# Kernel optimization log

Measured on AMD Instinct MI355X. Metric: run time of the kernel, lower is better.

Reference implementation:

```python
import jax, jax.numpy as jnp
import numpy as np

C = 64
INTER = C // 2  # 32
B, L = 4, 4096


def setup_inputs() -> dict:
    key = jax.random.key(0)
    ks = jax.random.split(key, 9)
    s_in = 1.0 / np.sqrt(C)
    s_inter = 1.0 / np.sqrt(INTER)
    return {
        "x": jax.random.normal(ks[0], (B, C, L), dtype=jnp.float32),
        "g_w": jax.random.normal(ks[1], (INTER, C), dtype=jnp.float32) * s_in,
        "g_b": jax.random.normal(ks[2], (INTER,), dtype=jnp.float32) * s_in,
        "theta_w": jax.random.normal(ks[3], (INTER, C), dtype=jnp.float32) * s_in,
        "theta_b": jax.random.normal(ks[4], (INTER,), dtype=jnp.float32) * s_in,
        "phi_w": jax.random.normal(ks[5], (INTER, C), dtype=jnp.float32) * s_in,
        "phi_b": jax.random.normal(ks[6], (INTER,), dtype=jnp.float32) * s_in,
        # NOTE: original inits W to zero (residual starts as identity); we use small
        # random values so the reference exercises the full computation.
        "W_w": jax.random.normal(ks[7], (C, INTER), dtype=jnp.float32) * s_inter,
        "W_b": jax.random.normal(ks[8], (C,), dtype=jnp.float32) * s_inter,
    }


def reference(x, g_w, g_b, theta_w, theta_b, phi_w, phi_b, W_w, W_b):
    # 1x1 Conv1d == channel matmul: [O,C] x [B,C,L] -> [B,O,L]
    g_x = jnp.einsum('oc,bcl->bol', g_w, x) + g_b[None, :, None]
    theta_x = jnp.einsum('oc,bcl->bol', theta_w, x) + theta_b[None, :, None]
    phi_x = jnp.einsum('oc,bcl->bol', phi_w, x) + phi_b[None, :, None]
    # f[b,l,m] = theta[:,l] . phi[:,m]  (unscaled attention scores, [B,L,L])
    f = jnp.einsum('bol,bom->blm', theta_x, phi_x)
    f_div_C = jax.nn.softmax(f, axis=-1)
    # y[b,o,l] = sum_m f[b,l,m] * g[b,o,m]
    y = jnp.einsum('blm,bom->bol', f_div_C, g_x)
    W_y = jnp.einsum('co,bol->bcl', W_w, y) + W_b[None, :, None]
    return W_y + x
```

## Files before the change

kernel.cpp:

```cpp
#include <hip/hip_runtime.h>

#define Bn 4
#define Cdim 64
#define INTER 32
#define Ln 4096
#define LOG2E 1.44269504088896340736f

typedef _Float16 half_t;
typedef __attribute__((ext_vector_type(8))) _Float16 half8v;
typedef __attribute__((ext_vector_type(4))) short short4v;
typedef __attribute__((ext_vector_type(8))) short short8v;
typedef __attribute__((ext_vector_type(4))) float f32x4;

__device__ __forceinline__ unsigned short f2bf(float f) {
    unsigned u = __float_as_uint(f);
    u += 0x7fffu + ((u >> 16) & 1u);
    return (unsigned short)(u >> 16);
}
__device__ __forceinline__ float bf2f(unsigned short b) {
    return __uint_as_float(((unsigned)b) << 16);
}
__device__ __forceinline__ unsigned pack_bf(float a, float b) {
    unsigned ua = __float_as_uint(a) + 0x8000u;
    unsigned ub = __float_as_uint(b) + 0x8000u;
    return __builtin_amdgcn_perm(ub, ua, 0x07060302);
}
__device__ __forceinline__ void gll16(const void* g, void* l) {
    __builtin_amdgcn_global_load_lds(
        (const __attribute__((address_space(1))) unsigned int*)g,
        (__attribute__((address_space(3))) unsigned int*)l, 16, 0, 0);
}

__global__ void setup_kernel(const float* __restrict__ g_w, const float* __restrict__ g_b,
                             const float* __restrict__ th_w, const float* __restrict__ th_b,
                             const float* __restrict__ ph_w, const float* __restrict__ ph_b,
                             const float* __restrict__ W_w, const float* __restrict__ W_b,
                             half_t* __restrict__ Wcat, float* __restrict__ biasbuf,
                             float* __restrict__ bc, half_t* __restrict__ Wm) {
    int blk = blockIdx.x, tid = threadIdx.x;
    if (blk < 96) {
        int row = blk;
        float v;
        if (row < 32) v = th_w[row * 64 + tid] * LOG2E;
        else if (row < 64) v = ph_w[(row - 32) * 64 + tid];
        else v = g_w[(row - 64) * 64 + tid];
        Wcat[row * 64 + tid] = (half_t)v;
    } else if (blk == 96) {
        for (int i = tid; i < 96; i += 64) {
            float v = (i < 32) ? th_b[i] * LOG2E : (i < 64) ? ph_b[i - 32] : g_b[i - 64];
            biasbuf[i] = v;
        }
    } else if (blk == 97) {
        bc[tid] = W_b[tid];
    } else {
        int l15 = tid & 15, jb = (tid >> 4) * 8;
        for (int mf = 0; mf < 4; mf++) {
            int c = mf * 16 + l15;
            half_t tmp[8];
            for (int j = 0; j < 8; j++) tmp[j] = (half_t)W_w[c * 32 + jb + j];
            float4 v;
            __builtin_memcpy(&v, tmp, 16);
            *(float4*)(Wm + (mf * 64 + tid) * 8) = v;
        }
    }
}

__global__ __launch_bounds__(192) void proj_kernel(
        const float* __restrict__ x, const half_t* __restrict__ Wcat,
        const float* __restrict__ biasbuf,
        half_t* __restrict__ thfrag, half_t* __restrict__ phfrag,
        unsigned short* __restrict__ gfrag) {
    __shared__ half_t sx[64][72];
    __shared__ unsigned short sg[2048];
    int tid = threadIdx.x;
    int b = blockIdx.x >> 6;
    int l0 = (blockIdx.x & 63) << 6;

    for (int i = tid; i < 1024; i += 192) {
        int c = i >> 4, lq = (i & 15) << 2;
        float4 v = *(const float4*)&x[(size_t)(b * 64 + c) * Ln + l0 + lq];
        sx[lq + 0][c] = (half_t)v.x;
        sx[lq + 1][c] = (half_t)v.y;
        sx[lq + 2][c] = (half_t)v.z;
        sx[lq + 3][c] = (half_t)v.w;
    }
    __syncthreads();

    int lane = tid & 63, grp = tid >> 6;
    int l15 = lane & 15, quad = lane >> 4;

    half8v wA[2][2];
#pragma unroll
    for (int mf = 0; mf < 2; mf++)
#pragma unroll
        for (int kk = 0; kk < 2; kk++)
            wA[mf][kk] = *(const half8v*)(Wcat + (grp * 32 + mf * 16 + l15) * 64 +
                                          kk * 32 + quad * 8);
    half8v xB[4][2];
#pragma unroll
    for (int nf = 0; nf < 4; nf++)
#pragma unroll
        for (int kk = 0; kk < 2; kk++)
            xB[nf][kk] = *(const half8v*)&sx[nf * 16 + l15][kk * 32 + quad * 8];

    f32x4 acc[2][4];
    const f32x4 z = {0.f, 0.f, 0.f, 0.f};
#pragma unroll
    for (int mf = 0; mf < 2; mf++)
#pragma unroll
        for (int nf = 0; nf < 4; nf++) {
            f32x4 a = __builtin_amdgcn_mfma_f32_16x16x32_f16(wA[mf][0], xB[nf][0], z, 0, 0, 0);
            acc[mf][nf] = __builtin_amdgcn_mfma_f32_16x16x32_f16(wA[mf][1], xB[nf][1], a, 0, 0, 0);
        }
#pragma unroll
    for (int mf = 0; mf < 2; mf++) {
        float4 bv = *(const float4*)&biasbuf[grp * 32 + mf * 16 + quad * 4];
#pragma unroll
        for (int nf = 0; nf < 4; nf++) {
            acc[mf][nf][0] += bv.x; acc[mf][nf][1] += bv.y;
            acc[mf][nf][2] += bv.z; acc[mf][nf][3] += bv.w;
        }
    }

    if (grp < 2) {
        half_t* F = (grp == 0) ? thfrag : phfrag;
#pragma unroll
        for (int mf = 0; mf < 2; mf++)
#pragma unroll
            for (int nf = 0; nf < 4; nf++) {
                half_t h[4];
                h[0] = (half_t)acc[mf][nf][0]; h[1] = (half_t)acc[mf][nf][1];
                h[2] = (half_t)acc[mf][nf][2]; h[3] = (half_t)acc[mf][nf][3];
                uint2 v;
                __builtin_memcpy(&v, h, 8);
                size_t u = (size_t)(b * 256 + (l0 >> 4) + nf) * 64 +
                           l15 + 16 * (mf * 2 + (quad >> 1));
                *(uint2*)(F + u * 8 + (quad & 1) * 4) = v;
            }
    } else {
#pragma unroll
        for (int mf = 0; mf < 2; mf++)
#pragma unroll
            for (int nf = 0; nf < 4; nf++)
#pragma unroll
                for (int r = 0; r < 4; r++) {
                    int lu = nf * 64 + (quad * 4 + r) + 16 * (l15 >> 2);
                    sg[lu * 8 + mf * 4 + (l15 & 3)] = f2bf(acc[mf][nf][r]);
                }
        __builtin_amdgcn_s_waitcnt(0);
        size_t base = (size_t)(b * 256 + (l0 >> 4)) * 512;
#pragma unroll
        for (int s = 0; s < 4; s++) {
            int i = lane + s * 64;
            uint4 v = ((const uint4*)sg)[i];
            *(uint4*)(gfrag + base + (size_t)i * 8) = v;
        }
    }
}

__global__ __launch_bounds__(256, 4) void attn_kernel(
        const half_t* __restrict__ thfrag, const half_t* __restrict__ phfrag,
        const unsigned short* __restrict__ gfrag,
        unsigned short* __restrict__ part, float* __restrict__ Sden,
        int KC, int CH) {
    __shared__ uint4 sbuf[2][512];

    int tid = threadIdx.x, lane = tid & 63, widx = tid >> 6;
    int l15 = lane & 15, quad = lane >> 4;

    int blk = blockIdx.x;
    int b = blk / (32 * KC);
    int rem = blk % (32 * KC);
    int qblk = rem / KC, kc = rem % KC;
    int qbase = qblk * 128 + widx * 32;
    int k0 = kc * CH;

    half8v th[2];
#pragma unroll
    for (int qf = 0; qf < 2; qf++)
        th[qf] = *(const half8v*)(thfrag +
                                  ((size_t)(b * 256 + (qbase >> 4) + qf) * 64 + lane) * 8);

    unsigned short oh = (l15 == 0) ? 0x3F80 : 0;
    short4v ones;
    ones[0] = (short)oh; ones[1] = (short)oh; ones[2] = (short)oh; ones[3] = (short)oh;

    f32x4 acc[2][2], accd[2];
#pragma unroll
    for (int qf = 0; qf < 2; qf++) {
        acc[qf][0] = (f32x4){0.f, 0.f, 0.f, 0.f};
        acc[qf][1] = (f32x4){0.f, 0.f, 0.f, 0.f};
        accd[qf]   = (f32x4){0.f, 0.f, 0.f, 0.f};
    }

    const char* phsrc = (const char*)(phfrag + (size_t)b * 256 * 512);
    const char* gsrc  = (const char*)(gfrag + (size_t)b * 256 * 512);
    const f32x4 z = {0.f, 0.f, 0.f, 0.f};

    gll16(phsrc + (size_t)(k0 >> 4) * 1024 + tid * 16, (char*)&sbuf[0][0] + tid * 16);
    gll16(gsrc + (size_t)(k0 >> 4) * 1024 + tid * 16, (char*)&sbuf[0][256] + tid * 16);
    __syncthreads();

    int cb = 0;
    for (int kt = k0; kt < k0 + CH; kt += 64) {
        if (kt + 64 < k0 + CH) {
            gll16(phsrc + (size_t)((kt + 64) >> 4) * 1024 + tid * 16,
                  (char*)&sbuf[cb ^ 1][0] + tid * 16);
            gll16(gsrc + (size_t)((kt + 64) >> 4) * 1024 + tid * 16,
                  (char*)&sbuf[cb ^ 1][256] + tid * 16);
        }
        const half_t* sph = (const half_t*)&sbuf[cb][0];
        const unsigned short* sg = (const unsigned short*)&sbuf[cb][256];
#pragma unroll
        for (int kf = 0; kf < 4; kf++) {
            half8v phA = *(const half8v*)(sph + kf * 512 + lane * 8);
            short8v g8 = *(const short8v*)(sg + kf * 512 + lane * 8);
            short4v ga0 = __builtin_shufflevector(g8, g8, 0, 1, 2, 3);
            short4v ga1 = __builtin_shufflevector(g8, g8, 4, 5, 6, 7);
#pragma unroll
            for (int qf = 0; qf < 2; qf++) {
                f32x4 s = __builtin_amdgcn_mfma_f32_16x16x32_f16(phA, th[qf], z, 0, 0, 0);
                float p0 = __builtin_amdgcn_exp2f(s[0]);
                float p1 = __builtin_amdgcn_exp2f(s[1]);
                float p2 = __builtin_amdgcn_exp2f(s[2]);
                float p3 = __builtin_amdgcn_exp2f(s[3]);
                union { short4v s4; uint2 u2; } pb;
                pb.u2.x = pack_bf(p0, p1);
                pb.u2.y = pack_bf(p2, p3);
                acc[qf][0] = __builtin_amdgcn_mfma_f32_16x16x16bf16_1k(ga0, pb.s4,
                                                                      acc[qf][0], 0, 0, 0);
                acc[qf][1] = __builtin_amdgcn_mfma_f32_16x16x16bf16_1k(ga1, pb.s4,
                                                                      acc[qf][1], 0, 0, 0);
                accd[qf] = __builtin_amdgcn_mfma_f32_16x16x16bf16_1k(ones, pb.s4,
                                                                    accd[qf], 0, 0, 0);
            }
        }
        __syncthreads();
        cb ^= 1;
    }

    size_t sb = (size_t)(b * KC + kc) * Ln + qbase;
    if (quad == 0) {
        Sden[sb + l15] = accd[0][0];
        Sden[sb + 16 + l15] = accd[1][0];
    }
    size_t pbase = (size_t)(b * KC + kc) * 32 * Ln;
#pragma unroll
    for (int qf = 0; qf < 2; qf++)
#pragma unroll
        for (int cf = 0; cf < 2; cf++)
#pragma unroll
            for (int r = 0; r < 4; r++) {
                int c = cf * 16 + quad * 4 + r;
                part[pbase + (size_t)c * Ln + qbase + qf * 16 + l15] =
                    f2bf(acc[qf][cf][r]);
            }
}

__global__ __launch_bounds__(256) void merge_kernel(
        const unsigned short* __restrict__ part, const float* __restrict__ Sden,
        const half_t* __restrict__ Wm, const float* __restrict__ bc,
        const float* __restrict__ x, float* __restrict__ out, int KC) {
    int tid = threadIdx.x, lane = tid & 63, widx = tid >> 6;
    int l15 = lane & 15, quad = lane >> 4;
    int b = blockIdx.x >> 6;
    int t16 = (blockIdx.x & 63) * 4 + widx;
    int l = (t16 << 4) + l15;

    float den = 0.f;
    for (int kc = 0; kc < KC; kc++) den += Sden[(size_t)(b * KC + kc) * Ln + l];
    float inv = 1.f / den;

    float num[8] = {0.f, 0.f, 0.f, 0.f, 0.f, 0.f, 0.f, 0.f};
    for (int kc = 0; kc < KC; kc++) {
        size_t base = ((size_t)((b * KC + kc) * 32) + quad * 8) * Ln + l;
#pragma unroll
        for (int j = 0; j < 8; j++) num[j] += bf2f(part[base + (size_t)j * Ln]);
    }
    half_t yh[8];
#pragma unroll
    for (int j = 0; j < 8; j++) yh[j] = (half_t)(num[j] * inv);
    half8v yB;
    __builtin_memcpy(&yB, yh, 16);

    const f32x4 z = {0.f, 0.f, 0.f, 0.f};
    f32x4 acc[4];
#pragma unroll
    for (int mf = 0; mf < 4; mf++) {
        half8v wA = *(const half8v*)(Wm + (mf * 64 + lane) * 8);
        acc[mf] = __builtin_amdgcn_mfma_f32_16x16x32_f16(wA, yB, z, 0, 0, 0);
    }
#pragma unroll
    for (int mf = 0; mf < 4; mf++) {
        float4 bv = *(const float4*)&bc[mf * 16 + quad * 4];
#pragma unroll
        for (int r = 0; r < 4; r++) {
            int c = mf * 16 + quad * 4 + r;
            size_t idx = (size_t)(b * 64 + c) * Ln + l;
            float bb = (r == 0) ? bv.x : (r == 1) ? bv.y : (r == 2) ? bv.z : bv.w;
            out[idx] = acc[mf][r] + bb + x[idx];
        }
    }
}

extern "C" void kernel_launch(void* const* d_in, const int* in_sizes, int n_in,
                              void* d_out, int out_size, void* d_ws, size_t ws_size,
                              hipStream_t stream) {
    const float* x    = (const float*)d_in[0];
    const float* g_w  = (const float*)d_in[1];
    const float* g_b  = (const float*)d_in[2];
    const float* th_w = (const float*)d_in[3];
    const float* th_b = (const float*)d_in[4];
    const float* ph_w = (const float*)d_in[5];
    const float* ph_b = (const float*)d_in[6];
    const float* W_w  = (const float*)d_in[7];
    const float* W_b  = (const float*)d_in[8];
    float* out = (float*)d_out;

    char* w = (char*)d_ws;
    const size_t off_th   = 0;
    const size_t off_ph   = 1048576;
    const size_t off_g    = 2097152;
    const size_t off_Wcat = 4194304;
    const size_t off_bias = 4206592;
    const size_t off_bc   = 4207104;
    const size_t off_Wm   = 4207360;
    const size_t off_Sden = 4211712;

    int KC = 8;
    size_t off_part = 0;
    while (true) {
        off_part = off_Sden + (size_t)KC * (Bn * Ln * 4);
        off_part = (off_part + 255) & ~(size_t)255;
        size_t need = off_part + (size_t)KC * ((size_t)Bn * 32 * Ln * 2);
        if (need <= ws_size || KC == 1) break;
        KC >>= 1;
    }

    half_t* thfrag = (half_t*)(w + off_th);
    half_t* phfrag = (half_t*)(w + off_ph);
    unsigned short* gfrag = (unsigned short*)(w + off_g);
    half_t* Wcat   = (half_t*)(w + off_Wcat);
    float* biasbuf = (float*)(w + off_bias);
    float* bc      = (float*)(w + off_bc);
    half_t* Wm     = (half_t*)(w + off_Wm);
    float* Sden    = (float*)(w + off_Sden);
    unsigned short* part = (unsigned short*)(w + off_part);

    int CH = Ln / KC;

    setup_kernel<<<99, 64, 0, stream>>>(g_w, g_b, th_w, th_b, ph_w, ph_b, W_w, W_b,
                                        Wcat, biasbuf, bc, Wm);
    proj_kernel<<<Bn * 64, 192, 0, stream>>>(x, Wcat, biasbuf, thfrag, phfrag, gfrag);
    attn_kernel<<<Bn * 32 * KC, 256, 0, stream>>>(thfrag, phfrag, gfrag, part, Sden,
                                                  KC, CH);
    merge_kernel<<<Bn * 64, 256, 0, stream>>>(part, Sden, Wm, bc, x, out, KC);
}
```

Before: 102.9 us.

## Drop setup kernel, shrink attention query tile, raise key split and occupancy

```diff
diff --git a/kernel.cpp b/kernel.cpp
--- a/kernel.cpp
+++ b/kernel.cpp
@@ -17,9 +17,6 @@
     u += 0x7fffu + ((u >> 16) & 1u);
     return (unsigned short)(u >> 16);
 }
-__device__ __forceinline__ float bf2f(unsigned short b) {
-    return __uint_as_float(((unsigned)b) << 16);
-}
 __device__ __forceinline__ unsigned pack_bf(float a, float b) {
     unsigned ua = __float_as_uint(a) + 0x8000u;
     unsigned ub = __float_as_uint(b) + 0x8000u;
@@ -30,44 +27,24 @@
         (const __attribute__((address_space(1))) unsigned int*)g,
         (__attribute__((address_space(3))) unsigned int*)l, 16, 0, 0);
 }
-
-__global__ void setup_kernel(const float* __restrict__ g_w, const float* __restrict__ g_b,
-                             const float* __restrict__ th_w, const float* __restrict__ th_b,
-                             const float* __restrict__ ph_w, const float* __restrict__ ph_b,
-                             const float* __restrict__ W_w, const float* __restrict__ W_b,
-                             half_t* __restrict__ Wcat, float* __restrict__ biasbuf,
-                             float* __restrict__ bc, half_t* __restrict__ Wm) {
-    int blk = blockIdx.x, tid = threadIdx.x;
-    if (blk < 96) {
-        int row = blk;
-        float v;
-        if (row < 32) v = th_w[row * 64 + tid] * LOG2E;
-        else if (row < 64) v = ph_w[(row - 32) * 64 + tid];
-        else v = g_w[(row - 64) * 64 + tid];
-        Wcat[row * 64 + tid] = (half_t)v;
-    } else if (blk == 96) {
-        for (int i = tid; i < 96; i += 64) {
-            float v = (i < 32) ? th_b[i] * LOG2E : (i < 64) ? ph_b[i - 32] : g_b[i - 64];
-            biasbuf[i] = v;
-        }
-    } else if (blk == 97) {
-        bc[tid] = W_b[tid];
-    } else {
-        int l15 = tid & 15, jb = (tid >> 4) * 8;
-        for (int mf = 0; mf < 4; mf++) {
-            int c = mf * 16 + l15;
-            half_t tmp[8];
-            for (int j = 0; j < 8; j++) tmp[j] = (half_t)W_w[c * 32 + jb + j];
-            float4 v;
-            __builtin_memcpy(&v, tmp, 16);
-            *(float4*)(Wm + (mf * 64 + tid) * 8) = v;
-        }
-    }
+__device__ __forceinline__ half8v cvt8(const float* p, float scale) {
+    float4 f0 = *(const float4*)p;
+    float4 f1 = *(const float4*)(p + 4);
+    half_t h[8];
+    h[0] = (half_t)(f0.x * scale); h[1] = (half_t)(f0.y * scale);
+    h[2] = (half_t)(f0.z * scale); h[3] = (half_t)(f0.w * scale);
+    h[4] = (half_t)(f1.x * scale); h[5] = (half_t)(f1.y * scale);
+    h[6] = (half_t)(f1.z * scale); h[7] = (half_t)(f1.w * scale);
+    half8v r;
+    __builtin_memcpy(&r, h, 16);
+    return r;
 }
 
 __global__ __launch_bounds__(192) void proj_kernel(
-        const float* __restrict__ x, const half_t* __restrict__ Wcat,
-        const float* __restrict__ biasbuf,
+        const float* __restrict__ x,
+        const float* __restrict__ g_w, const float* __restrict__ g_b,
+        const float* __restrict__ th_w, const float* __restrict__ th_b,
+        const float* __restrict__ ph_w, const float* __restrict__ ph_b,
         half_t* __restrict__ thfrag, half_t* __restrict__ phfrag,
         unsigned short* __restrict__ gfrag) {
     __shared__ half_t sx[64][72];
@@ -89,13 +66,16 @@
     int lane = tid & 63, grp = tid >> 6;
     int l15 = lane & 15, quad = lane >> 4;
 
+    const float* Wsrc = (grp == 0) ? th_w : (grp == 1) ? ph_w : g_w;
+    const float* bsrc = (grp == 0) ? th_b : (grp == 1) ? ph_b : g_b;
+    float scale = (grp == 0) ? LOG2E : 1.0f;
+
     half8v wA[2][2];
 #pragma unroll
     for (int mf = 0; mf < 2; mf++)
 #pragma unroll
         for (int kk = 0; kk < 2; kk++)
-            wA[mf][kk] = *(const half8v*)(Wcat + (grp * 32 + mf * 16 + l15) * 64 +
-                                          kk * 32 + quad * 8);
+            wA[mf][kk] = cvt8(&Wsrc[(mf * 16 + l15) * 64 + kk * 32 + quad * 8], scale);
     half8v xB[4][2];
 #pragma unroll
     for (int nf = 0; nf < 4; nf++)
@@ -114,11 +94,12 @@
         }
 #pragma unroll
     for (int mf = 0; mf < 2; mf++) {
-        float4 bv = *(const float4*)&biasbuf[grp * 32 + mf * 16 + quad * 4];
+        float4 bv = *(const float4*)&bsrc[mf * 16 + quad * 4];
+        float s0 = bv.x * scale, s1 = bv.y * scale, s2 = bv.z * scale, s3 = bv.w * scale;
 #pragma unroll
         for (int nf = 0; nf < 4; nf++) {
-            acc[mf][nf][0] += bv.x; acc[mf][nf][1] += bv.y;
-            acc[mf][nf][2] += bv.z; acc[mf][nf][3] += bv.w;
+            acc[mf][nf][0] += s0; acc[mf][nf][1] += s1;
+            acc[mf][nf][2] += s2; acc[mf][nf][3] += s3;
         }
     }
 
@@ -158,7 +139,7 @@
     }
 }
 
-__global__ __launch_bounds__(256, 4) void attn_kernel(
+__global__ __launch_bounds__(256, 8) void attn_kernel(
         const half_t* __restrict__ thfrag, const half_t* __restrict__ phfrag,
         const unsigned short* __restrict__ gfrag,
         unsigned short* __restrict__ part, float* __restrict__ Sden,
@@ -169,29 +150,22 @@
     int l15 = lane & 15, quad = lane >> 4;
 
     int blk = blockIdx.x;
-    int b = blk / (32 * KC);
-    int rem = blk % (32 * KC);
+    int b = blk / (64 * KC);
+    int rem = blk % (64 * KC);
     int qblk = rem / KC, kc = rem % KC;
-    int qbase = qblk * 128 + widx * 32;
+    int qbase = qblk * 64 + widx * 16;
     int k0 = kc * CH;
 
-    half8v th[2];
-#pragma unroll
-    for (int qf = 0; qf < 2; qf++)
-        th[qf] = *(const half8v*)(thfrag +
-                                  ((size_t)(b * 256 + (qbase >> 4) + qf) * 64 + lane) * 8);
+    half8v th = *(const half8v*)(thfrag +
+                                 ((size_t)(b * 256 + qblk * 4 + widx) * 64 + lane) * 8);
 
     unsigned short oh = (l15 == 0) ? 0x3F80 : 0;
     short4v ones;
     ones[0] = (short)oh; ones[1] = (short)oh; ones[2] = (short)oh; ones[3] = (short)oh;
 
-    f32x4 acc[2][2], accd[2];
-#pragma unroll
-    for (int qf = 0; qf < 2; qf++) {
-        acc[qf][0] = (f32x4){0.f, 0.f, 0.f, 0.f};
-        acc[qf][1] = (f32x4){0.f, 0.f, 0.f, 0.f};
-        accd[qf]   = (f32x4){0.f, 0.f, 0.f, 0.f};
-    }
+    f32x4 acc0 = {0.f, 0.f, 0.f, 0.f};
+    f32x4 acc1 = {0.f, 0.f, 0.f, 0.f};
+    f32x4 accd = {0.f, 0.f, 0.f, 0.f};
 
     const char* phsrc = (const char*)(phfrag + (size_t)b * 256 * 512);
     const char* gsrc  = (const char*)(gfrag + (size_t)b * 256 * 512);
@@ -217,49 +191,40 @@
             short8v g8 = *(const short8v*)(sg + kf * 512 + lane * 8);
             short4v ga0 = __builtin_shufflevector(g8, g8, 0, 1, 2, 3);
             short4v ga1 = __builtin_shufflevector(g8, g8, 4, 5, 6, 7);
-#pragma unroll
-            for (int qf = 0; qf < 2; qf++) {
-                f32x4 s = __builtin_amdgcn_mfma_f32_16x16x32_f16(phA, th[qf], z, 0, 0, 0);
-                float p0 = __builtin_amdgcn_exp2f(s[0]);
-                float p1 = __builtin_amdgcn_exp2f(s[1]);
-                float p2 = __builtin_amdgcn_exp2f(s[2]);
-                float p3 = __builtin_amdgcn_exp2f(s[3]);
-                union { short4v s4; uint2 u2; } pb;
-                pb.u2.x = pack_bf(p0, p1);
-                pb.u2.y = pack_bf(p2, p3);
-                acc[qf][0] = __builtin_amdgcn_mfma_f32_16x16x16bf16_1k(ga0, pb.s4,
-                                                                      acc[qf][0], 0, 0, 0);
-                acc[qf][1] = __builtin_amdgcn_mfma_f32_16x16x16bf16_1k(ga1, pb.s4,
-                                                                      acc[qf][1], 0, 0, 0);
-                accd[qf] = __builtin_amdgcn_mfma_f32_16x16x16bf16_1k(ones, pb.s4,
-                                                                    accd[qf], 0, 0, 0);
-            }
+            f32x4 s = __builtin_amdgcn_mfma_f32_16x16x32_f16(phA, th, z, 0, 0, 0);
+            float p0 = __builtin_amdgcn_exp2f(s[0]);
+            float p1 = __builtin_amdgcn_exp2f(s[1]);
+            float p2 = __builtin_amdgcn_exp2f(s[2]);
+            float p3 = __builtin_amdgcn_exp2f(s[3]);
+            union { short4v s4; uint2 u2; } pb;
+            pb.u2.x = pack_bf(p0, p1);
+            pb.u2.y = pack_bf(p2, p3);
+            acc0 = __builtin_amdgcn_mfma_f32_16x16x16bf16_1k(ga0, pb.s4, acc0, 0, 0, 0);
+            acc1 = __builtin_amdgcn_mfma_f32_16x16x16bf16_1k(ga1, pb.s4, acc1, 0, 0, 0);
+            accd = __builtin_amdgcn_mfma_f32_16x16x16bf16_1k(ones, pb.s4, accd, 0, 0, 0);
         }
         __syncthreads();
         cb ^= 1;
     }
 
-    size_t sb = (size_t)(b * KC + kc) * Ln + qbase;
-    if (quad == 0) {
-        Sden[sb + l15] = accd[0][0];
-        Sden[sb + 16 + l15] = accd[1][0];
-    }
-    size_t pbase = (size_t)(b * KC + kc) * 32 * Ln;
-#pragma unroll
-    for (int qf = 0; qf < 2; qf++)
-#pragma unroll
-        for (int cf = 0; cf < 2; cf++)
-#pragma unroll
-            for (int r = 0; r < 4; r++) {
-                int c = cf * 16 + quad * 4 + r;
-                part[pbase + (size_t)c * Ln + qbase + qf * 16 + l15] =
-                    f2bf(acc[qf][cf][r]);
-            }
+    if (quad == 0) Sden[(size_t)(b * KC + kc) * Ln + qbase + l15] = accd[0];
+
+    unsigned short* tbuf = (unsigned short*)&sbuf[0][0] + widx * 640;
+    *(unsigned*)&tbuf[l15 * 40 + quad * 4]      = pack_bf(acc0[0], acc0[1]);
+    *(unsigned*)&tbuf[l15 * 40 + quad * 4 + 2]  = pack_bf(acc0[2], acc0[3]);
+    *(unsigned*)&tbuf[l15 * 40 + 16 + quad * 4]     = pack_bf(acc1[0], acc1[1]);
+    *(unsigned*)&tbuf[l15 * 40 + 16 + quad * 4 + 2] = pack_bf(acc1[2], acc1[3]);
+    __syncthreads();
+    {
+        int ql = lane >> 2, cq = (lane & 3) * 8;
+        uint4 v = *(const uint4*)&tbuf[ql * 40 + cq];
+        *(uint4*)(part + ((size_t)(b * KC + kc) * Ln + qbase + ql) * 32 + cq) = v;
+    }
 }
 
 __global__ __launch_bounds__(256) void merge_kernel(
         const unsigned short* __restrict__ part, const float* __restrict__ Sden,
-        const half_t* __restrict__ Wm, const float* __restrict__ bc,
+        const float* __restrict__ W_w, const float* __restrict__ W_b,
         const float* __restrict__ x, float* __restrict__ out, int KC) {
     int tid = threadIdx.x, lane = tid & 63, widx = tid >> 6;
     int l15 = lane & 15, quad = lane >> 4;
@@ -273,9 +238,13 @@
 
     float num[8] = {0.f, 0.f, 0.f, 0.f, 0.f, 0.f, 0.f, 0.f};
     for (int kc = 0; kc < KC; kc++) {
-        size_t base = ((size_t)((b * KC + kc) * 32) + quad * 8) * Ln + l;
-#pragma unroll
-        for (int j = 0; j < 8; j++) num[j] += bf2f(part[base + (size_t)j * Ln]);
+        uint4 v = *(const uint4*)&part[((size_t)(b * KC + kc) * Ln + l) * 32 + quad * 8];
+        unsigned vv[4] = {v.x, v.y, v.z, v.w};
+#pragma unroll
+        for (int t = 0; t < 4; t++) {
+            num[2 * t]     += __uint_as_float(vv[t] << 16);
+            num[2 * t + 1] += __uint_as_float(vv[t] & 0xffff0000u);
+        }
     }
     half_t yh[8];
 #pragma unroll
@@ -287,12 +256,12 @@
     f32x4 acc[4];
 #pragma unroll
     for (int mf = 0; mf < 4; mf++) {
-        half8v wA = *(const half8v*)(Wm + (mf * 64 + lane) * 8);
+        half8v wA = cvt8(&W_w[(mf * 16 + l15) * 32 + quad * 8], 1.0f);
         acc[mf] = __builtin_amdgcn_mfma_f32_16x16x32_f16(wA, yB, z, 0, 0, 0);
     }
 #pragma unroll
     for (int mf = 0; mf < 4; mf++) {
-        float4 bv = *(const float4*)&bc[mf * 16 + quad * 4];
+        float4 bv = *(const float4*)&W_b[mf * 16 + quad * 4];
 #pragma unroll
         for (int r = 0; r < 4; r++) {
             int c = mf * 16 + quad * 4 + r;
@@ -321,18 +290,14 @@
     const size_t off_th   = 0;
     const size_t off_ph   = 1048576;
     const size_t off_g    = 2097152;
-    const size_t off_Wcat = 4194304;
-    const size_t off_bias = 4206592;
-    const size_t off_bc   = 4207104;
-    const size_t off_Wm   = 4207360;
-    const size_t off_Sden = 4211712;
-
-    int KC = 8;
+    const size_t off_Sden = 3145728;
+
+    int KC = 16;
     size_t off_part = 0;
     while (true) {
         off_part = off_Sden + (size_t)KC * (Bn * Ln * 4);
         off_part = (off_part + 255) & ~(size_t)255;
-        size_t need = off_part + (size_t)KC * ((size_t)Bn * 32 * Ln * 2);
+        size_t need = off_part + (size_t)KC * ((size_t)Bn * Ln * 32 * 2);
         if (need <= ws_size || KC == 1) break;
         KC >>= 1;
     }
@@ -340,19 +305,14 @@
     half_t* thfrag = (half_t*)(w + off_th);
     half_t* phfrag = (half_t*)(w + off_ph);
     unsigned short* gfrag = (unsigned short*)(w + off_g);
-    half_t* Wcat   = (half_t*)(w + off_Wcat);
-    float* biasbuf = (float*)(w + off_bias);
-    float* bc      = (float*)(w + off_bc);
-    half_t* Wm     = (half_t*)(w + off_Wm);
     float* Sden    = (float*)(w + off_Sden);
     unsigned short* part = (unsigned short*)(w + off_part);
 
     int CH = Ln / KC;
 
-    setup_kernel<<<99, 64, 0, stream>>>(g_w, g_b, th_w, th_b, ph_w, ph_b, W_w, W_b,
-                                        Wcat, biasbuf, bc, Wm);
-    proj_kernel<<<Bn * 64, 192, 0, stream>>>(x, Wcat, biasbuf, thfrag, phfrag, gfrag);
-    attn_kernel<<<Bn * 32 * KC, 256, 0, stream>>>(thfrag, phfrag, gfrag, part, Sden,
+    proj_kernel<<<Bn * 64, 192, 0, stream>>>(x, g_w, g_b, th_w, th_b, ph_w, ph_b,
+                                             thfrag, phfrag, gfrag);
+    attn_kernel<<<Bn * 64 * KC, 256, 0, stream>>>(thfrag, phfrag, gfrag, part, Sden,
                                                   KC, CH);
-    merge_kernel<<<Bn * 64, 256, 0, stream>>>(part, Sden, Wm, bc, x, out, KC);
-}
+    merge_kernel<<<Bn * 64, 256, 0, stream>>>(part, Sden, W_w, W_b, x, out, KC);
+}
```

Result: slower. 106.2 us (+3.2%).
